# Kernel tuning notes

Measured on AMD Instinct MI355X. Metric: run time of the kernel, lower is better.

The kernel has to match this reference:

```python
import jax, jax.numpy as jnp
import numpy as np

NMS_THRESH = 0.5
SCORE_THRESH = 0.2
MAX_SUBJECT = 15
MAX_OBJECT = 15
B, NS, NO = 32, 512, 512


def _make_boxes(k, b, n):
    u = jax.random.uniform(k, (b, n, 4))
    xy = u[..., :2] * 1000.0          # top-left corner
    wh = u[..., 2:] * 200.0 + 1.0     # positive width/height
    return jnp.concatenate([xy, xy + wh], axis=-1)  # valid xyxy boxes


def setup_inputs() -> dict:
    key = jax.random.key(0)
    ks = jax.random.split(key, 6)
    return {
        "subj_boxes": _make_boxes(ks[0], B, NS),
        "subj_scores": jax.random.uniform(ks[1], (B, NS)),
        "subj_labels": jax.random.randint(ks[2], (B, NS), 0, 30, dtype=jnp.int32),
        "obj_boxes": _make_boxes(ks[3], B, NO),
        "obj_scores": jax.random.uniform(ks[4], (B, NO)),
        "obj_labels": jax.random.randint(ks[5], (B, NO), 0, 30, dtype=jnp.int32),
    }


def reference(subj_boxes, subj_scores, subj_labels, obj_boxes, obj_scores, obj_labels):
    # concat subject + object detections per image, as in preprocess()
    boxes = jnp.concatenate([subj_boxes, obj_boxes], axis=1)    # [B,N,4]
    scores = jnp.concatenate([subj_scores, obj_scores], axis=1) # [B,N]
    labels = jnp.concatenate([subj_labels, obj_labels], axis=1) # [B,N]
    b, n = scores.shape
    is_subj = jnp.arange(n) < subj_boxes.shape[1]               # [N]

    # sort by score descending (matches the argsort after NMS; greedy NMS
    # preserves this ordering among survivors)
    order = jnp.argsort(-scores, axis=1)
    boxes = jnp.take_along_axis(boxes, order[..., None], axis=1)
    scores = jnp.take_along_axis(scores, order, axis=1)
    labels = jnp.take_along_axis(labels, order, axis=1)
    is_subj = jnp.take(is_subj, order)                          # [B,N]

    active = scores >= SCORE_THRESH

    # torchvision batched_nms: offset boxes per class so distinct classes
    # never overlap (comparisons only -> no gradient path)
    max_coord = jax.lax.stop_gradient(jnp.max(boxes))
    ob = boxes + labels.astype(boxes.dtype)[..., None] * (max_coord + 1.0)

    # pairwise IoU [B,N,N]
    area = (ob[..., 2] - ob[..., 0]) * (ob[..., 3] - ob[..., 1])
    lt = jnp.maximum(ob[:, :, None, :2], ob[:, None, :, :2])
    rb = jnp.minimum(ob[:, :, None, 2:], ob[:, None, :, 2:])
    wh = jnp.clip(rb - lt, 0.0)
    inter = wh[..., 0] * wh[..., 1]
    iou = inter / (area[:, :, None] + area[:, None, :] - inter)

    later = jnp.arange(n)[None, :] > jnp.arange(n)[:, None]     # strictly lower-score

    def body(i, suppressed):  # greedy NMS, vectorized over batch
        keep_i = active[:, i] & ~suppressed[:, i]
        return suppressed | (keep_i[:, None] & (iou[:, i, :] > NMS_THRESH) & later[i])

    suppressed = jax.lax.fori_loop(0, n, body, jnp.zeros((b, n), dtype=bool))
    kept = active & ~suppressed

    # split survivors into subjects / objects, keep top max_subject/max_object
    neg = jnp.finfo(scores.dtype).min
    sub_key = jnp.where(kept & is_subj, scores, neg)
    obj_key = jnp.where(kept & ~is_subj, scores, neg)
    sv, si = jax.lax.top_k(sub_key, MAX_SUBJECT)
    ov, oi = jax.lax.top_k(obj_key, MAX_OBJECT)
    idx = jnp.concatenate([si, oi], axis=1)                     # [B,K]
    valid = jnp.concatenate([sv, ov], axis=1) > neg             # [B,K]

    out_boxes = jnp.take_along_axis(boxes, idx[..., None], axis=1) * valid[..., None]
    out_scores = jnp.take_along_axis(scores, idx, axis=1) * valid
    out_labels = jnp.where(valid, jnp.take_along_axis(labels, idx, axis=1), -1)
    num_subjects = jnp.sum(sv > neg, axis=1)
    return out_boxes, out_scores, out_labels, num_subjects, valid
```

## Files before the change

kernel.cpp:

```cpp
#include <hip/hip_runtime.h>
#include <stdint.h>

#define BQ    32
#define NSUB  512
#define NDET  1024
#define NCLS  30
#define KSLOT 30
#define CAP   128

#pragma clang fp contract(off)

typedef unsigned long long u64;

__global__ __launch_bounds__(1024) void max_kernel(
    const float4* __restrict__ sb4, const float4* __restrict__ ob4,
    unsigned* __restrict__ wsmax)
{
    int t = blockIdx.x * 1024 + threadIdx.x;
    float4 a = sb4[t], b = ob4[t];
    float m = fmaxf(fmaxf(fmaxf(a.x, a.y), fmaxf(a.z, a.w)),
                    fmaxf(fmaxf(b.x, b.y), fmaxf(b.z, b.w)));
    for (int off = 32; off; off >>= 1) m = fmaxf(m, __shfl_xor(m, off));
    if ((threadIdx.x & 63) == 0) atomicMax(wsmax, __float_as_uint(m));
}

__global__ __launch_bounds__(64) void nms_class_kernel(
    const float* __restrict__ sb, const float* __restrict__ ss,
    const int*   __restrict__ sl,
    const float* __restrict__ ob, const float* __restrict__ os,
    const int*   __restrict__ ol,
    const unsigned* __restrict__ wsmax,
    u64* __restrict__ subk, u64* __restrict__ objk)
{
#pragma clang fp contract(off)
    const int c    = blockIdx.x;
    const int b    = blockIdx.y;
    const int lane = threadIdx.x;

    __shared__ u64    keyarr[CAP];
    __shared__ u64    skey[CAP];
    __shared__ float4 bx4[CAP];

    const float mco  = __uint_as_float(wsmax[0]) + 1.0f;
    const float offc = (float)c * mco;

    int cnt = 0;
    for (int base = 0; base < NDET; base += 64) {
        int i = base + lane;
        float sc; int lb;
        if (i < NSUB) { sc = ss[b * NSUB + i];        lb = sl[b * NSUB + i]; }
        else          { sc = os[b * NSUB + i - NSUB]; lb = ol[b * NSUB + i - NSUB]; }
        bool pred = (lb == c) && (sc >= 0.2f);
        u64 mb = __ballot(pred);
        if (pred) {
            int pos = cnt + (int)__popcll(mb & ((1ull << lane) - 1ull));
            if (pos < CAP)
                keyarr[pos] = ((u64)__float_as_uint(sc) << 32) | (u64)(1023 - i);
        }
        cnt += (int)__popcll(mb);
    }
    if (cnt > CAP) cnt = CAP;
    __syncthreads();

    {
        u64 K = (lane < cnt) ? keyarr[lane] : 0;
        int r = 0;
        for (int l = 0; l < cnt; ++l) r += (keyarr[l] > K) ? 1 : 0;
        if (lane < cnt) skey[r] = K;
    }
    if (cnt > 64) {
        int e = 64 + lane;
        u64 K = (e < cnt) ? keyarr[e] : 0;
        int r = 0;
        for (int l = 0; l < cnt; ++l) r += (keyarr[l] > K) ? 1 : 0;
        if (e < cnt) skey[r] = K;
    }
    __syncthreads();

    const int lim1 = (cnt < 64) ? cnt : 64;
    const bool have1 = (lane < lim1);
    u64 SK1 = have1 ? skey[lane] : 0;
    int idx1 = 1023 - (int)(unsigned)(SK1 & 0xffffffffull);
    float4 bj1 = make_float4(0.f, 0.f, 0.f, 0.f);
    if (have1) {
        bj1 = (idx1 < NSUB)
            ? *(const float4*)(sb + (size_t)(b * NSUB + idx1) * 4)
            : *(const float4*)(ob + (size_t)(b * NSUB + idx1 - NSUB) * 4);
        bx4[lane] = bj1;
    }
    const bool have2 = (64 + lane) < cnt;
    u64 SK2 = 0; int idx2 = 0; float4 bj2 = make_float4(0.f, 0.f, 0.f, 0.f);
    if (cnt > 64) {
        SK2 = have2 ? skey[64 + lane] : 0;
        idx2 = 1023 - (int)(unsigned)(SK2 & 0xffffffffull);
        if (have2) {
            bj2 = (idx2 < NSUB)
                ? *(const float4*)(sb + (size_t)(b * NSUB + idx2) * 4)
                : *(const float4*)(ob + (size_t)(b * NSUB + idx2 - NSUB) * 4);
            bx4[64 + lane] = bj2;
        }
    }
    __syncthreads();

    float j0 = bj1.x + offc, j1 = bj1.y + offc, j2v = bj1.z + offc, j3 = bj1.w + offc;
    float aj = (j2v - j0) * (j3 - j1);
    u64 ov = 0;
    for (int l = 0; l < lim1; ++l) {
        float4 bl = bx4[l];
        float i0 = bl.x + offc, i1 = bl.y + offc, i2 = bl.z + offc, i3 = bl.w + offc;
        float ai = (i2 - i0) * (i3 - i1);
        if (have1 && l < lane) {
            float ltx = fmaxf(i0, j0), lty = fmaxf(i1, j1);
            float rbx = fminf(i2, j2v), rby = fminf(i3, j3);
            float wx = fmaxf(rbx - ltx, 0.0f), wy = fmaxf(rby - lty, 0.0f);
            float inter = wx * wy;
            float iou = inter / ((ai + aj) - inter);
            if (iou > 0.5f) ov |= (1ull << l);
        }
    }
    bool sup1 = !have1;
    for (int l = 0; l < lim1; ++l) {
        u64 bal = __ballot(sup1);
        if (!((bal >> l) & 1ull)) sup1 = sup1 || (((ov >> l) & 1ull) != 0ull);
    }
    const bool kept1 = have1 && !sup1;
    const u64 keptA = __ballot(kept1);

    bool kept2 = false;
    if (cnt > 64) {
        float k0 = bj2.x + offc, k1 = bj2.y + offc, k2 = bj2.z + offc, k3 = bj2.w + offc;
        float ak = (k2 - k0) * (k3 - k1);
        bool sup2 = !have2;
        for (int l = 0; l < 64; ++l) {
            if ((keptA >> l) & 1ull) {
                float4 bl = bx4[l];
                float i0 = bl.x + offc, i1 = bl.y + offc, i2 = bl.z + offc, i3 = bl.w + offc;
                float ai = (i2 - i0) * (i3 - i1);
                if (!sup2) {
                    float ltx = fmaxf(i0, k0), lty = fmaxf(i1, k1);
                    float rbx = fminf(i2, k2), rby = fminf(i3, k3);
                    float wx = fmaxf(rbx - ltx, 0.0f), wy = fmaxf(rby - lty, 0.0f);
                    float inter = wx * wy;
                    float iou = inter / ((ai + ak) - inter);
                    if (iou > 0.5f) sup2 = true;
                }
            }
        }
        u64 ov2 = 0;
        const int lim2 = cnt - 64;
        for (int l = 0; l < lim2; ++l) {
            float4 bl = bx4[64 + l];
            float i0 = bl.x + offc, i1 = bl.y + offc, i2 = bl.z + offc, i3 = bl.w + offc;
            float ai = (i2 - i0) * (i3 - i1);
            if (have2 && l < lane) {
                float ltx = fmaxf(i0, k0), lty = fmaxf(i1, k1);
                float rbx = fminf(i2, k2), rby = fminf(i3, k3);
                float wx = fmaxf(rbx - ltx, 0.0f), wy = fmaxf(rby - lty, 0.0f);
                float inter = wx * wy;
                float iou = inter / ((ai + ak) - inter);
                if (iou > 0.5f) ov2 |= (1ull << l);
            }
        }
        for (int l = 0; l < lim2; ++l) {
            u64 bal = __ballot(sup2);
            if (!((bal >> l) & 1ull)) sup2 = sup2 || (((ov2 >> l) & 1ull) != 0ull);
        }
        kept2 = have2 && !sup2;
    }

    const bool s1 = kept1 && (idx1 < NSUB), o1 = kept1 && (idx1 >= NSUB);
    const bool s2 = kept2 && (idx2 < NSUB), o2 = kept2 && (idx2 >= NSUB);
    const u64 mS1 = __ballot(s1), mS2 = __ballot(s2);
    const u64 mO1 = __ballot(o1), mO2 = __ballot(o2);
    const u64 ltm = (1ull << lane) - 1ull;
    u64* subp = subk + ((size_t)b * NCLS + c) * 15;
    u64* objp = objk + ((size_t)b * NCLS + c) * 15;
    if (s1) { int p = (int)__popcll(mS1 & ltm); if (p < 15) subp[p] = SK1; }
    if (s2) { int p = (int)__popcll(mS1) + (int)__popcll(mS2 & ltm); if (p < 15) subp[p] = SK2; }
    if (o1) { int p = (int)__popcll(mO1 & ltm); if (p < 15) objp[p] = SK1; }
    if (o2) { int p = (int)__popcll(mO1) + (int)__popcll(mO2 & ltm); if (p < 15) objp[p] = SK2; }
    int tS = (int)(__popcll(mS1) + __popcll(mS2)); if (tS > 15) tS = 15;
    int tO = (int)(__popcll(mO1) + __popcll(mO2)); if (tO > 15) tO = 15;
    if (lane >= tS && lane < 15) subp[lane] = 0;
    if (lane >= tO && lane < 15) objp[lane] = 0;
}

__global__ __launch_bounds__(512) void select_kernel(
    const float* __restrict__ sb, const float* __restrict__ ss,
    const int*   __restrict__ sl,
    const float* __restrict__ ob, const float* __restrict__ os,
    const int*   __restrict__ ol,
    const u64* __restrict__ subk, const u64* __restrict__ objk,
    float* __restrict__ out)
{
    const int b    = blockIdx.x;
    const int side = blockIdx.y;
    const int t    = threadIdx.x;
    __shared__ u64 ks[512];

    const u64* src = side ? objk : subk;
    u64 K = (t < NCLS * 15) ? src[(size_t)b * NCLS * 15 + t] : 0;

    for (unsigned k = 2; k <= 512; k <<= 1) {
        for (unsigned j = k >> 1; j > 0; j >>= 1) {
            bool want_max = (((t & k) == 0) == ((t & j) == 0));
            u64 other;
            if (j >= 64) {
                ks[t] = K; __syncthreads();
                other = ks[t ^ j]; __syncthreads();
            } else {
                other = __shfl_xor(K, (int)j);
            }
            bool take = want_max ? (other > K) : (other < K);
            if (take) K = other;
        }
    }

    float* outB = out;
    float* outS = out + BQ * KSLOT * 4;
    float* outL = outS + BQ * KSLOT;
    float* outN = outL + BQ * KSLOT;
    float* outV = outN + BQ;

    if (t < 15) {
        int p = b * KSLOT + (side ? (15 + t) : t);
        if (K != 0) {
            int idx = 1023 - (int)(unsigned)(K & 0xffffffffull);
            float score = __uint_as_float((unsigned)(K >> 32));
            float4 bx; int lb;
            if (idx < NSUB) {
                bx = *(const float4*)(sb + (size_t)(b * NSUB + idx) * 4);
                lb = sl[b * NSUB + idx];
            } else {
                bx = *(const float4*)(ob + (size_t)(b * NSUB + idx - NSUB) * 4);
                lb = ol[b * NSUB + idx - NSUB];
            }
            *(float4*)(outB + (size_t)p * 4) = bx;
            outS[p] = score;
            outL[p] = (float)lb;
            outV[p] = 1.0f;
        } else {
            *(float4*)(outB + (size_t)p * 4) = make_float4(0.f, 0.f, 0.f, 0.f);
            outS[p] = 0.0f;
            outL[p] = -1.0f;
            outV[p] = 0.0f;
        }
    }
    if (side == 0 && t < 64) {
        u64 mvalid = __ballot((t < 15) && (K != 0));
        if (t == 0) outN[b] = (float)__popcll(mvalid);
    }
}

extern "C" void kernel_launch(void* const* d_in, const int* in_sizes, int n_in,
                              void* d_out, int out_size, void* d_ws, size_t ws_size,
                              hipStream_t stream) {
    const float* sb = (const float*)d_in[0];
    const float* ss = (const float*)d_in[1];
    const int*   sl = (const int*)d_in[2];
    const float* ob = (const float*)d_in[3];
    const float* os = (const float*)d_in[4];
    const int*   ol = (const int*)d_in[5];

    unsigned* wsmax = (unsigned*)d_ws;
    u64* subk = (u64*)((char*)d_ws + 16);
    u64* objk = subk + (size_t)BQ * NCLS * 15;

    hipMemsetAsync(d_ws, 0, 16, stream);
    max_kernel<<<dim3(16), dim3(1024), 0, stream>>>(
        (const float4*)sb, (const float4*)ob, wsmax);
    nms_class_kernel<<<dim3(NCLS, BQ), dim3(64), 0, stream>>>(
        sb, ss, sl, ob, os, ol, wsmax, subk, objk);
    select_kernel<<<dim3(BQ, 2), dim3(512), 0, stream>>>(
        sb, ss, sl, ob, os, ol, subk, objk, (float*)d_out);
}
```

Measured before the change: 94.54 us.

## Fuse max, per-class NMS and top-k select into one per-image kernel

Replaces the memset and three kernels (global max, per-class NMS, bitonic select) with a single kernel of one 512-thread block per image. Each block recomputes the global box maximum redundantly, then its 8 wavefronts each handle classes in a strided loop, keeping candidates in shared memory before the bitonic top-k. This removes launch overhead and the global workspace round trip. In exchange, only 32 blocks run, each rereading all boxes for the max, and each wavefront processes about 4 classes serially, so parallelism drops.

```diff
diff --git a/kernel.cpp b/kernel.cpp
--- a/kernel.cpp
+++ b/kernel.cpp
@@ -7,214 +7,199 @@
 #define NCLS  30
 #define KSLOT 30
 #define CAP   128
+#define NTH   512
 
 #pragma clang fp contract(off)
 
 typedef unsigned long long u64;
 
-__global__ __launch_bounds__(1024) void max_kernel(
-    const float4* __restrict__ sb4, const float4* __restrict__ ob4,
-    unsigned* __restrict__ wsmax)
-{
-    int t = blockIdx.x * 1024 + threadIdx.x;
-    float4 a = sb4[t], b = ob4[t];
-    float m = fmaxf(fmaxf(fmaxf(a.x, a.y), fmaxf(a.z, a.w)),
-                    fmaxf(fmaxf(b.x, b.y), fmaxf(b.z, b.w)));
-    for (int off = 32; off; off >>= 1) m = fmaxf(m, __shfl_xor(m, off));
-    if ((threadIdx.x & 63) == 0) atomicMax(wsmax, __float_as_uint(m));
-}
-
-__global__ __launch_bounds__(64) void nms_class_kernel(
+__global__ __launch_bounds__(NTH) void fused_kernel(
     const float* __restrict__ sb, const float* __restrict__ ss,
     const int*   __restrict__ sl,
     const float* __restrict__ ob, const float* __restrict__ os,
     const int*   __restrict__ ol,
-    const unsigned* __restrict__ wsmax,
-    u64* __restrict__ subk, u64* __restrict__ objk)
+    float* __restrict__ out)
 {
 #pragma clang fp contract(off)
-    const int c    = blockIdx.x;
-    const int b    = blockIdx.y;
-    const int lane = threadIdx.x;
-
-    __shared__ u64    keyarr[CAP];
-    __shared__ u64    skey[CAP];
-    __shared__ float4 bx4[CAP];
-
-    const float mco  = __uint_as_float(wsmax[0]) + 1.0f;
-    const float offc = (float)c * mco;
-
-    int cnt = 0;
-    for (int base = 0; base < NDET; base += 64) {
-        int i = base + lane;
-        float sc; int lb;
-        if (i < NSUB) { sc = ss[b * NSUB + i];        lb = sl[b * NSUB + i]; }
-        else          { sc = os[b * NSUB + i - NSUB]; lb = ol[b * NSUB + i - NSUB]; }
-        bool pred = (lb == c) && (sc >= 0.2f);
-        u64 mb = __ballot(pred);
-        if (pred) {
-            int pos = cnt + (int)__popcll(mb & ((1ull << lane) - 1ull));
-            if (pos < CAP)
-                keyarr[pos] = ((u64)__float_as_uint(sc) << 32) | (u64)(1023 - i);
-        }
-        cnt += (int)__popcll(mb);
+    const int b    = blockIdx.x;
+    const int t    = threadIdx.x;
+    const int lane = t & 63;
+    const int w    = t >> 6;
+
+    __shared__ float  red[8];
+    __shared__ u64    keyarr[8][CAP];
+    __shared__ u64    skey[8][CAP];
+    __shared__ float4 bxw[8][CAP];
+    __shared__ u64    subcand[NTH];
+    __shared__ u64    objcand[NTH];
+    __shared__ u64    ks[NTH];
+
+    float m = 0.0f;
+    const float4* sb4 = (const float4*)sb;
+    const float4* ob4 = (const float4*)ob;
+    for (int i = t; i < BQ * NSUB; i += NTH) {
+        float4 a = sb4[i], c4 = ob4[i];
+        m = fmaxf(m, fmaxf(fmaxf(a.x, a.y), fmaxf(a.z, a.w)));
+        m = fmaxf(m, fmaxf(fmaxf(c4.x, c4.y), fmaxf(c4.z, c4.w)));
     }
-    if (cnt > CAP) cnt = CAP;
+    for (int off = 32; off; off >>= 1) m = fmaxf(m, __shfl_xor(m, off));
+    if (lane == 0) red[w] = m;
+    subcand[t] = 0;
+    objcand[t] = 0;
     __syncthreads();
-
-    {
-        u64 K = (lane < cnt) ? keyarr[lane] : 0;
-        int r = 0;
-        for (int l = 0; l < cnt; ++l) r += (keyarr[l] > K) ? 1 : 0;
-        if (lane < cnt) skey[r] = K;
-    }
-    if (cnt > 64) {
-        int e = 64 + lane;
-        u64 K = (e < cnt) ? keyarr[e] : 0;
-        int r = 0;
-        for (int l = 0; l < cnt; ++l) r += (keyarr[l] > K) ? 1 : 0;
-        if (e < cnt) skey[r] = K;
-    }
-    __syncthreads();
-
-    const int lim1 = (cnt < 64) ? cnt : 64;
-    const bool have1 = (lane < lim1);
-    u64 SK1 = have1 ? skey[lane] : 0;
-    int idx1 = 1023 - (int)(unsigned)(SK1 & 0xffffffffull);
-    float4 bj1 = make_float4(0.f, 0.f, 0.f, 0.f);
-    if (have1) {
-        bj1 = (idx1 < NSUB)
-            ? *(const float4*)(sb + (size_t)(b * NSUB + idx1) * 4)
-            : *(const float4*)(ob + (size_t)(b * NSUB + idx1 - NSUB) * 4);
-        bx4[lane] = bj1;
-    }
-    const bool have2 = (64 + lane) < cnt;
-    u64 SK2 = 0; int idx2 = 0; float4 bj2 = make_float4(0.f, 0.f, 0.f, 0.f);
-    if (cnt > 64) {
-        SK2 = have2 ? skey[64 + lane] : 0;
-        idx2 = 1023 - (int)(unsigned)(SK2 & 0xffffffffull);
-        if (have2) {
-            bj2 = (idx2 < NSUB)
-                ? *(const float4*)(sb + (size_t)(b * NSUB + idx2) * 4)
-                : *(const float4*)(ob + (size_t)(b * NSUB + idx2 - NSUB) * 4);
-            bx4[64 + lane] = bj2;
-        }
-    }
-    __syncthreads();
-
-    float j0 = bj1.x + offc, j1 = bj1.y + offc, j2v = bj1.z + offc, j3 = bj1.w + offc;
-    float aj = (j2v - j0) * (j3 - j1);
-    u64 ov = 0;
-    for (int l = 0; l < lim1; ++l) {
-        float4 bl = bx4[l];
-        float i0 = bl.x + offc, i1 = bl.y + offc, i2 = bl.z + offc, i3 = bl.w + offc;
-        float ai = (i2 - i0) * (i3 - i1);
-        if (have1 && l < lane) {
-            float ltx = fmaxf(i0, j0), lty = fmaxf(i1, j1);
-            float rbx = fminf(i2, j2v), rby = fminf(i3, j3);
-            float wx = fmaxf(rbx - ltx, 0.0f), wy = fmaxf(rby - lty, 0.0f);
-            float inter = wx * wy;
-            float iou = inter / ((ai + aj) - inter);
-            if (iou > 0.5f) ov |= (1ull << l);
-        }
-    }
-    bool sup1 = !have1;
-    for (int l = 0; l < lim1; ++l) {
-        u64 bal = __ballot(sup1);
-        if (!((bal >> l) & 1ull)) sup1 = sup1 || (((ov >> l) & 1ull) != 0ull);
-    }
-    const bool kept1 = have1 && !sup1;
-    const u64 keptA = __ballot(kept1);
-
-    bool kept2 = false;
-    if (cnt > 64) {
-        float k0 = bj2.x + offc, k1 = bj2.y + offc, k2 = bj2.z + offc, k3 = bj2.w + offc;
-        float ak = (k2 - k0) * (k3 - k1);
-        bool sup2 = !have2;
-        for (int l = 0; l < 64; ++l) {
-            if ((keptA >> l) & 1ull) {
-                float4 bl = bx4[l];
-                float i0 = bl.x + offc, i1 = bl.y + offc, i2 = bl.z + offc, i3 = bl.w + offc;
+    float mm = red[0];
+    for (int i = 1; i < 8; ++i) mm = fmaxf(mm, red[i]);
+    const float mco = mm + 1.0f;
+
+    for (int c = w; c < NCLS; c += 8) {
+        u64*    KA = keyarr[w];
+        u64*    SK = skey[w];
+        float4* BX = bxw[w];
+        const float offc = (float)c * mco;
+
+        int cnt = 0;
+        for (int base = 0; base < NDET; base += 64) {
+            int i = base + lane;
+            float scv; int lb;
+            if (i < NSUB) { scv = ss[b * NSUB + i];        lb = sl[b * NSUB + i]; }
+            else          { scv = os[b * NSUB + i - NSUB]; lb = ol[b * NSUB + i - NSUB]; }
+            bool pred = (lb == c) && (scv >= 0.2f);
+            u64 mb = __ballot(pred);
+            if (pred) {
+                int pos = cnt + (int)__popcll(mb & ((1ull << lane) - 1ull));
+                if (pos < CAP)
+                    KA[pos] = ((u64)__float_as_uint(scv) << 32) | (u64)(1023 - i);
+            }
+            cnt += (int)__popcll(mb);
+        }
+        if (cnt > CAP) cnt = CAP;
+        __threadfence_block();
+
+        {
+            u64 K = (lane < cnt) ? KA[lane] : 0;
+            int r = 0;
+            for (int l = 0; l < cnt; ++l) r += (KA[l] > K) ? 1 : 0;
+            if (lane < cnt) SK[r] = K;
+        }
+        if (cnt > 64) {
+            int e = 64 + lane;
+            u64 K = (e < cnt) ? KA[e] : 0;
+            int r = 0;
+            for (int l = 0; l < cnt; ++l) r += (KA[l] > K) ? 1 : 0;
+            if (e < cnt) SK[r] = K;
+        }
+        __threadfence_block();
+
+        const int  lim1  = (cnt < 64) ? cnt : 64;
+        const bool have1 = (lane < lim1);
+        u64 SK1 = have1 ? SK[lane] : 0;
+        int idx1 = 1023 - (int)(unsigned)(SK1 & 0xffffffffull);
+        float4 bj1 = make_float4(0.f, 0.f, 0.f, 0.f);
+        if (have1) {
+            bj1 = (idx1 < NSUB)
+                ? *(const float4*)(sb + (size_t)(b * NSUB + idx1) * 4)
+                : *(const float4*)(ob + (size_t)(b * NSUB + idx1 - NSUB) * 4);
+            BX[lane] = bj1;
+        }
+        const bool have2 = (64 + lane) < cnt;
+        u64 SK2 = 0; int idx2 = 0; float4 bj2 = make_float4(0.f, 0.f, 0.f, 0.f);
+        if (cnt > 64) {
+            SK2 = have2 ? SK[64 + lane] : 0;
+            idx2 = 1023 - (int)(unsigned)(SK2 & 0xffffffffull);
+            if (have2) {
+                bj2 = (idx2 < NSUB)
+                    ? *(const float4*)(sb + (size_t)(b * NSUB + idx2) * 4)
+                    : *(const float4*)(ob + (size_t)(b * NSUB + idx2 - NSUB) * 4);
+                BX[64 + lane] = bj2;
+            }
+        }
+        __threadfence_block();
+
+        float j0 = bj1.x + offc, j1 = bj1.y + offc;
+        float j2v = bj1.z + offc, j3 = bj1.w + offc;
+        float aj = (j2v - j0) * (j3 - j1);
+        u64 ov = 0;
+        for (int l = 0; l < lim1; ++l) {
+            float4 bl = BX[l];
+            float i0 = bl.x + offc, i1 = bl.y + offc;
+            float i2 = bl.z + offc, i3 = bl.w + offc;
+            float ai = (i2 - i0) * (i3 - i1);
+            if (have1 && l < lane) {
+                float ltx = fmaxf(i0, j0), lty = fmaxf(i1, j1);
+                float rbx = fminf(i2, j2v), rby = fminf(i3, j3);
+                float wx = fmaxf(rbx - ltx, 0.0f), wy = fmaxf(rby - lty, 0.0f);
+                float inter = wx * wy;
+                float iou = inter / ((ai + aj) - inter);
+                if (iou > 0.5f) ov |= (1ull << l);
+            }
+        }
+        bool sup1 = !have1;
+        for (int l = 0; l < lim1; ++l) {
+            u64 bal = __ballot(sup1);
+            if (!((bal >> l) & 1ull)) sup1 = sup1 || (((ov >> l) & 1ull) != 0ull);
+        }
+        const bool kept1 = have1 && !sup1;
+        const u64 keptA = __ballot(kept1);
+
+        bool kept2 = false;
+        if (cnt > 64) {
+            float k0 = bj2.x + offc, k1 = bj2.y + offc;
+            float k2 = bj2.z + offc, k3 = bj2.w + offc;
+            float ak = (k2 - k0) * (k3 - k1);
+            bool sup2 = !have2;
+            for (int l = 0; l < 64; ++l) {
+                if ((keptA >> l) & 1ull) {
+                    float4 bl = BX[l];
+                    float i0 = bl.x + offc, i1 = bl.y + offc;
+                    float i2 = bl.z + offc, i3 = bl.w + offc;
+                    float ai = (i2 - i0) * (i3 - i1);
+                    if (!sup2) {
+                        float ltx = fmaxf(i0, k0), lty = fmaxf(i1, k1);
+                        float rbx = fminf(i2, k2), rby = fminf(i3, k3);
+                        float wx = fmaxf(rbx - ltx, 0.0f), wy = fmaxf(rby - lty, 0.0f);
+                        float inter = wx * wy;
+                        float iou = inter / ((ai + ak) - inter);
+                        if (iou > 0.5f) sup2 = true;
+                    }
+                }
+            }
+            u64 ov2 = 0;
+            const int lim2 = cnt - 64;
+            for (int l = 0; l < lim2; ++l) {
+                float4 bl = BX[64 + l];
+                float i0 = bl.x + offc, i1 = bl.y + offc;
+                float i2 = bl.z + offc, i3 = bl.w + offc;
                 float ai = (i2 - i0) * (i3 - i1);
-                if (!sup2) {
+                if (have2 && l < lane) {
                     float ltx = fmaxf(i0, k0), lty = fmaxf(i1, k1);
                     float rbx = fminf(i2, k2), rby = fminf(i3, k3);
                     float wx = fmaxf(rbx - ltx, 0.0f), wy = fmaxf(rby - lty, 0.0f);
                     float inter = wx * wy;
                     float iou = inter / ((ai + ak) - inter);
-                    if (iou > 0.5f) sup2 = true;
-                }
-            }
-        }
-        u64 ov2 = 0;
-        const int lim2 = cnt - 64;
-        for (int l = 0; l < lim2; ++l) {
-            float4 bl = bx4[64 + l];
-            float i0 = bl.x + offc, i1 = bl.y + offc, i2 = bl.z + offc, i3 = bl.w + offc;
-            float ai = (i2 - i0) * (i3 - i1);
-            if (have2 && l < lane) {
-                float ltx = fmaxf(i0, k0), lty = fmaxf(i1, k1);
-                float rbx = fminf(i2, k2), rby = fminf(i3, k3);
-                float wx = fmaxf(rbx - ltx, 0.0f), wy = fmaxf(rby - lty, 0.0f);
-                float inter = wx * wy;
-                float iou = inter / ((ai + ak) - inter);
-                if (iou > 0.5f) ov2 |= (1ull << l);
-            }
-        }
-        for (int l = 0; l < lim2; ++l) {
-            u64 bal = __ballot(sup2);
-            if (!((bal >> l) & 1ull)) sup2 = sup2 || (((ov2 >> l) & 1ull) != 0ull);
-        }
-        kept2 = have2 && !sup2;
+                    if (iou > 0.5f) ov2 |= (1ull << l);
+                }
+            }
+            for (int l = 0; l < lim2; ++l) {
+                u64 bal = __ballot(sup2);
+                if (!((bal >> l) & 1ull)) sup2 = sup2 || (((ov2 >> l) & 1ull) != 0ull);
+            }
+            kept2 = have2 && !sup2;
+        }
+
+        const bool s1 = kept1 && (idx1 < NSUB), o1 = kept1 && (idx1 >= NSUB);
+        const bool s2 = kept2 && (idx2 < NSUB), o2 = kept2 && (idx2 >= NSUB);
+        const u64 mS1 = __ballot(s1), mS2 = __ballot(s2);
+        const u64 mO1 = __ballot(o1), mO2 = __ballot(o2);
+        const u64 ltm = (1ull << lane) - 1ull;
+        u64* subp = subcand + c * 15;
+        u64* objp = objcand + c * 15;
+        if (s1) { int p = (int)__popcll(mS1 & ltm); if (p < 15) subp[p] = SK1; }
+        if (s2) { int p = (int)__popcll(mS1) + (int)__popcll(mS2 & ltm); if (p < 15) subp[p] = SK2; }
+        if (o1) { int p = (int)__popcll(mO1 & ltm); if (p < 15) objp[p] = SK1; }
+        if (o2) { int p = (int)__popcll(mO1) + (int)__popcll(mO2 & ltm); if (p < 15) objp[p] = SK2; }
+        __threadfence_block();
     }
-
-    const bool s1 = kept1 && (idx1 < NSUB), o1 = kept1 && (idx1 >= NSUB);
-    const bool s2 = kept2 && (idx2 < NSUB), o2 = kept2 && (idx2 >= NSUB);
-    const u64 mS1 = __ballot(s1), mS2 = __ballot(s2);
-    const u64 mO1 = __ballot(o1), mO2 = __ballot(o2);
-    const u64 ltm = (1ull << lane) - 1ull;
-    u64* subp = subk + ((size_t)b * NCLS + c) * 15;
-    u64* objp = objk + ((size_t)b * NCLS + c) * 15;
-    if (s1) { int p = (int)__popcll(mS1 & ltm); if (p < 15) subp[p] = SK1; }
-    if (s2) { int p = (int)__popcll(mS1) + (int)__popcll(mS2 & ltm); if (p < 15) subp[p] = SK2; }
-    if (o1) { int p = (int)__popcll(mO1 & ltm); if (p < 15) objp[p] = SK1; }
-    if (o2) { int p = (int)__popcll(mO1) + (int)__popcll(mO2 & ltm); if (p < 15) objp[p] = SK2; }
-    int tS = (int)(__popcll(mS1) + __popcll(mS2)); if (tS > 15) tS = 15;
-    int tO = (int)(__popcll(mO1) + __popcll(mO2)); if (tO > 15) tO = 15;
-    if (lane >= tS && lane < 15) subp[lane] = 0;
-    if (lane >= tO && lane < 15) objp[lane] = 0;
-}
-
-__global__ __launch_bounds__(512) void select_kernel(
-    const float* __restrict__ sb, const float* __restrict__ ss,
-    const int*   __restrict__ sl,
-    const float* __restrict__ ob, const float* __restrict__ os,
-    const int*   __restrict__ ol,
-    const u64* __restrict__ subk, const u64* __restrict__ objk,
-    float* __restrict__ out)
-{
-    const int b    = blockIdx.x;
-    const int side = blockIdx.y;
-    const int t    = threadIdx.x;
-    __shared__ u64 ks[512];
-
-    const u64* src = side ? objk : subk;
-    u64 K = (t < NCLS * 15) ? src[(size_t)b * NCLS * 15 + t] : 0;
-
-    for (unsigned k = 2; k <= 512; k <<= 1) {
-        for (unsigned j = k >> 1; j > 0; j >>= 1) {
-            bool want_max = (((t & k) == 0) == ((t & j) == 0));
-            u64 other;
-            if (j >= 64) {
-                ks[t] = K; __syncthreads();
-                other = ks[t ^ j]; __syncthreads();
-            } else {
-                other = __shfl_xor(K, (int)j);
-            }
-            bool take = want_max ? (other > K) : (other < K);
-            if (take) K = other;
-        }
-    }
+    __syncthreads();
 
     float* outB = out;
     float* outS = out + BQ * KSLOT * 4;
@@ -222,33 +207,52 @@
     float* outN = outL + BQ * KSLOT;
     float* outV = outN + BQ;
 
-    if (t < 15) {
-        int p = b * KSLOT + (side ? (15 + t) : t);
-        if (K != 0) {
-            int idx = 1023 - (int)(unsigned)(K & 0xffffffffull);
-            float score = __uint_as_float((unsigned)(K >> 32));
-            float4 bx; int lb;
-            if (idx < NSUB) {
-                bx = *(const float4*)(sb + (size_t)(b * NSUB + idx) * 4);
-                lb = sl[b * NSUB + idx];
+    for (int side = 0; side < 2; ++side) {
+        u64 K = side ? objcand[t] : subcand[t];
+        for (unsigned k = 2; k <= NTH; k <<= 1) {
+            for (unsigned j = k >> 1; j > 0; j >>= 1) {
+                bool want_max = (((t & k) == 0) == ((t & j) == 0));
+                u64 other;
+                if (j >= 64) {
+                    ks[t] = K; __syncthreads();
+                    other = ks[t ^ j]; __syncthreads();
+                } else {
+                    other = __shfl_xor(K, (int)j);
+                }
+                bool take = want_max ? (other > K) : (other < K);
+                if (take) K = other;
+            }
+        }
+
+        if (t < 15) {
+            int p = b * KSLOT + (side ? (15 + t) : t);
+            if (K != 0) {
+                int idx = 1023 - (int)(unsigned)(K & 0xffffffffull);
+                float score = __uint_as_float((unsigned)(K >> 32));
+                float4 bx; int lb;
+                if (idx < NSUB) {
+                    bx = *(const float4*)(sb + (size_t)(b * NSUB + idx) * 4);
+                    lb = sl[b * NSUB + idx];
+                } else {
+                    bx = *(const float4*)(ob + (size_t)(b * NSUB + idx - NSUB) * 4);
+                    lb = ol[b * NSUB + idx - NSUB];
+                }
+                *(float4*)(outB + (size_t)p * 4) = bx;
+                outS[p] = score;
+                outL[p] = (float)lb;
+                outV[p] = 1.0f;
             } else {
-                bx = *(const float4*)(ob + (size_t)(b * NSUB + idx - NSUB) * 4);
-                lb = ol[b * NSUB + idx - NSUB];
-            }
-            *(float4*)(outB + (size_t)p * 4) = bx;
-            outS[p] = score;
-            outL[p] = (float)lb;
-            outV[p] = 1.0f;
-        } else {
-            *(float4*)(outB + (size_t)p * 4) = make_float4(0.f, 0.f, 0.f, 0.f);
-            outS[p] = 0.0f;
-            outL[p] = -1.0f;
-            outV[p] = 0.0f;
-        }
-    }
-    if (side == 0 && t < 64) {
-        u64 mvalid = __ballot((t < 15) && (K != 0));
-        if (t == 0) outN[b] = (float)__popcll(mvalid);
+                *(float4*)(outB + (size_t)p * 4) = make_float4(0.f, 0.f, 0.f, 0.f);
+                outS[p] = 0.0f;
+                outL[p] = -1.0f;
+                outV[p] = 0.0f;
+            }
+        }
+        if (side == 0 && t < 64) {
+            u64 mvalid = __ballot((t < 15) && (K != 0));
+            if (t == 0) outN[b] = (float)__popcll(mvalid);
+        }
+        __syncthreads();
     }
 }
 
@@ -261,16 +265,6 @@
     const float* ob = (const float*)d_in[3];
     const float* os = (const float*)d_in[4];
     const int*   ol = (const int*)d_in[5];
-
-    unsigned* wsmax = (unsigned*)d_ws;
-    u64* subk = (u64*)((char*)d_ws + 16);
-    u64* objk = subk + (size_t)BQ * NCLS * 15;
-
-    hipMemsetAsync(d_ws, 0, 16, stream);
-    max_kernel<<<dim3(16), dim3(1024), 0, stream>>>(
-        (const float4*)sb, (const float4*)ob, wsmax);
-    nms_class_kernel<<<dim3(NCLS, BQ), dim3(64), 0, stream>>>(
-        sb, ss, sl, ob, os, ol, wsmax, subk, objk);
-    select_kernel<<<dim3(BQ, 2), dim3(512), 0, stream>>>(
-        sb, ss, sl, ob, os, ol, subk, objk, (float*)d_out);
+    fused_kernel<<<dim3(BQ), dim3(NTH), 0, stream>>>(
+        sb, ss, sl, ob, os, ol, (float*)d_out);
 }
```

Result: slower. 121.4 us (+28.4%).

## Fuse top-k selection into NMS kernel via last-block atomic counter

Applied to the files above, without the earlier changes.

Drops the separate memset and select kernel. The max kernel now writes per-block partial maxima and resets per-image counters. The NMS kernel folds those partials itself, and the last class block to finish for each image does a wave-level iterative top-15 selection in place of the 512-thread bitonic sort. This removes two launches and a sort, at the cost of one atomic and a threadfence per block and a serial selection done by one wavefront per image.

```diff
diff --git a/kernel.cpp b/kernel.cpp
--- a/kernel.cpp
+++ b/kernel.cpp
@@ -14,14 +14,22 @@
 
 __global__ __launch_bounds__(1024) void max_kernel(
     const float4* __restrict__ sb4, const float4* __restrict__ ob4,
-    unsigned* __restrict__ wsmax)
+    float* __restrict__ pmax, int* __restrict__ done)
 {
-    int t = blockIdx.x * 1024 + threadIdx.x;
+    __shared__ float red[16];
+    const int t = blockIdx.x * 1024 + threadIdx.x;
     float4 a = sb4[t], b = ob4[t];
     float m = fmaxf(fmaxf(fmaxf(a.x, a.y), fmaxf(a.z, a.w)),
                     fmaxf(fmaxf(b.x, b.y), fmaxf(b.z, b.w)));
     for (int off = 32; off; off >>= 1) m = fmaxf(m, __shfl_xor(m, off));
-    if ((threadIdx.x & 63) == 0) atomicMax(wsmax, __float_as_uint(m));
+    if ((threadIdx.x & 63) == 0) red[threadIdx.x >> 6] = m;
+    __syncthreads();
+    if (threadIdx.x == 0) {
+        float mm = red[0];
+        for (int i = 1; i < 16; ++i) mm = fmaxf(mm, red[i]);
+        pmax[blockIdx.x] = mm;
+    }
+    if (blockIdx.x == 0 && threadIdx.x < BQ) done[threadIdx.x] = 0;
 }
 
 __global__ __launch_bounds__(64) void nms_class_kernel(
@@ -29,8 +37,9 @@
     const int*   __restrict__ sl,
     const float* __restrict__ ob, const float* __restrict__ os,
     const int*   __restrict__ ol,
-    const unsigned* __restrict__ wsmax,
-    u64* __restrict__ subk, u64* __restrict__ objk)
+    const float* __restrict__ pmax, int* __restrict__ done,
+    u64* __restrict__ subk, u64* __restrict__ objk,
+    float* __restrict__ out)
 {
 #pragma clang fp contract(off)
     const int c    = blockIdx.x;
@@ -41,7 +50,9 @@
     __shared__ u64    skey[CAP];
     __shared__ float4 bx4[CAP];
 
-    const float mco  = __uint_as_float(wsmax[0]) + 1.0f;
+    float mm = pmax[0];
+    for (int i = 1; i < 16; ++i) mm = fmaxf(mm, pmax[i]);
+    const float mco  = mm + 1.0f;
     const float offc = (float)c * mco;
 
     int cnt = 0;
@@ -77,7 +88,7 @@
     }
     __syncthreads();
 
-    const int lim1 = (cnt < 64) ? cnt : 64;
+    const int  lim1  = (cnt < 64) ? cnt : 64;
     const bool have1 = (lane < lim1);
     u64 SK1 = have1 ? skey[lane] : 0;
     int idx1 = 1023 - (int)(unsigned)(SK1 & 0xffffffffull);
@@ -102,12 +113,14 @@
     }
     __syncthreads();
 
-    float j0 = bj1.x + offc, j1 = bj1.y + offc, j2v = bj1.z + offc, j3 = bj1.w + offc;
+    float j0 = bj1.x + offc, j1 = bj1.y + offc;
+    float j2v = bj1.z + offc, j3 = bj1.w + offc;
     float aj = (j2v - j0) * (j3 - j1);
     u64 ov = 0;
     for (int l = 0; l < lim1; ++l) {
         float4 bl = bx4[l];
-        float i0 = bl.x + offc, i1 = bl.y + offc, i2 = bl.z + offc, i3 = bl.w + offc;
+        float i0 = bl.x + offc, i1 = bl.y + offc;
+        float i2 = bl.z + offc, i3 = bl.w + offc;
         float ai = (i2 - i0) * (i3 - i1);
         if (have1 && l < lane) {
             float ltx = fmaxf(i0, j0), lty = fmaxf(i1, j1);
@@ -128,13 +141,15 @@
 
     bool kept2 = false;
     if (cnt > 64) {
-        float k0 = bj2.x + offc, k1 = bj2.y + offc, k2 = bj2.z + offc, k3 = bj2.w + offc;
+        float k0 = bj2.x + offc, k1 = bj2.y + offc;
+        float k2 = bj2.z + offc, k3 = bj2.w + offc;
         float ak = (k2 - k0) * (k3 - k1);
         bool sup2 = !have2;
         for (int l = 0; l < 64; ++l) {
             if ((keptA >> l) & 1ull) {
                 float4 bl = bx4[l];
-                float i0 = bl.x + offc, i1 = bl.y + offc, i2 = bl.z + offc, i3 = bl.w + offc;
+                float i0 = bl.x + offc, i1 = bl.y + offc;
+                float i2 = bl.z + offc, i3 = bl.w + offc;
                 float ai = (i2 - i0) * (i3 - i1);
                 if (!sup2) {
                     float ltx = fmaxf(i0, k0), lty = fmaxf(i1, k1);
@@ -150,7 +165,8 @@
         const int lim2 = cnt - 64;
         for (int l = 0; l < lim2; ++l) {
             float4 bl = bx4[64 + l];
-            float i0 = bl.x + offc, i1 = bl.y + offc, i2 = bl.z + offc, i3 = bl.w + offc;
+            float i0 = bl.x + offc, i1 = bl.y + offc;
+            float i2 = bl.z + offc, i3 = bl.w + offc;
             float ai = (i2 - i0) * (i3 - i1);
             if (have2 && l < lane) {
                 float ltx = fmaxf(i0, k0), lty = fmaxf(i1, k1);
@@ -183,38 +199,14 @@
     int tO = (int)(__popcll(mO1) + __popcll(mO2)); if (tO > 15) tO = 15;
     if (lane >= tS && lane < 15) subp[lane] = 0;
     if (lane >= tO && lane < 15) objp[lane] = 0;
-}
-
-__global__ __launch_bounds__(512) void select_kernel(
-    const float* __restrict__ sb, const float* __restrict__ ss,
-    const int*   __restrict__ sl,
-    const float* __restrict__ ob, const float* __restrict__ os,
-    const int*   __restrict__ ol,
-    const u64* __restrict__ subk, const u64* __restrict__ objk,
-    float* __restrict__ out)
-{
-    const int b    = blockIdx.x;
-    const int side = blockIdx.y;
-    const int t    = threadIdx.x;
-    __shared__ u64 ks[512];
-
-    const u64* src = side ? objk : subk;
-    u64 K = (t < NCLS * 15) ? src[(size_t)b * NCLS * 15 + t] : 0;
-
-    for (unsigned k = 2; k <= 512; k <<= 1) {
-        for (unsigned j = k >> 1; j > 0; j >>= 1) {
-            bool want_max = (((t & k) == 0) == ((t & j) == 0));
-            u64 other;
-            if (j >= 64) {
-                ks[t] = K; __syncthreads();
-                other = ks[t ^ j]; __syncthreads();
-            } else {
-                other = __shfl_xor(K, (int)j);
-            }
-            bool take = want_max ? (other > K) : (other < K);
-            if (take) K = other;
-        }
-    }
+
+    __threadfence();
+    int old = 0;
+    if (lane == 0) old = atomicAdd(&done[b], 1);
+    old = __shfl(old, 0);
+    if (old != NCLS - 1) return;
+
+    __threadfence();
 
     float* outB = out;
     float* outS = out + BQ * KSLOT * 4;
@@ -222,33 +214,57 @@
     float* outN = outL + BQ * KSLOT;
     float* outV = outN + BQ;
 
-    if (t < 15) {
-        int p = b * KSLOT + (side ? (15 + t) : t);
-        if (K != 0) {
-            int idx = 1023 - (int)(unsigned)(K & 0xffffffffull);
-            float score = __uint_as_float((unsigned)(K >> 32));
-            float4 bx; int lb;
-            if (idx < NSUB) {
-                bx = *(const float4*)(sb + (size_t)(b * NSUB + idx) * 4);
-                lb = sl[b * NSUB + idx];
+    const u64* sk_im = subk + (size_t)b * NCLS * 15;
+    const u64* ok_im = objk + (size_t)b * NCLS * 15;
+
+    for (int side = 0; side < 2; ++side) {
+        const u64* src = side ? ok_im : sk_im;
+        u64 kk[8];
+        #pragma unroll
+        for (int i = 0; i < 8; ++i) {
+            int p = lane + 64 * i;
+            kk[i] = (p < NCLS * 15) ? src[p] : 0;
+        }
+        int nvalid = 0;
+        for (int r = 0; r < 15; ++r) {
+            u64 lm = 0; int li = 0;
+            #pragma unroll
+            for (int i = 0; i < 8; ++i) if (kk[i] > lm) { lm = kk[i]; li = i; }
+            u64 gm = lm;
+            for (int off = 32; off; off >>= 1) {
+                u64 o = __shfl_xor(gm, off);
+                if (o > gm) gm = o;
+            }
+            int p = b * KSLOT + (side ? (15 + r) : r);
+            if (gm == 0) {
+                if (lane == 0) {
+                    *(float4*)(outB + (size_t)p * 4) = make_float4(0.f, 0.f, 0.f, 0.f);
+                    outS[p] = 0.0f; outL[p] = -1.0f; outV[p] = 0.0f;
+                }
             } else {
-                bx = *(const float4*)(ob + (size_t)(b * NSUB + idx - NSUB) * 4);
-                lb = ol[b * NSUB + idx - NSUB];
-            }
-            *(float4*)(outB + (size_t)p * 4) = bx;
-            outS[p] = score;
-            outL[p] = (float)lb;
-            outV[p] = 1.0f;
-        } else {
-            *(float4*)(outB + (size_t)p * 4) = make_float4(0.f, 0.f, 0.f, 0.f);
-            outS[p] = 0.0f;
-            outL[p] = -1.0f;
-            outV[p] = 0.0f;
-        }
-    }
-    if (side == 0 && t < 64) {
-        u64 mvalid = __ballot((t < 15) && (K != 0));
-        if (t == 0) outN[b] = (float)__popcll(mvalid);
+                u64 win = __ballot(lm == gm);
+                int wl = (int)__ffsll(win) - 1;
+                if (lane == wl) {
+                    kk[li] = 0;
+                    int idx = 1023 - (int)(unsigned)(gm & 0xffffffffull);
+                    float score = __uint_as_float((unsigned)(gm >> 32));
+                    float4 bx; int lb;
+                    if (idx < NSUB) {
+                        bx = *(const float4*)(sb + (size_t)(b * NSUB + idx) * 4);
+                        lb = sl[b * NSUB + idx];
+                    } else {
+                        bx = *(const float4*)(ob + (size_t)(b * NSUB + idx - NSUB) * 4);
+                        lb = ol[b * NSUB + idx - NSUB];
+                    }
+                    *(float4*)(outB + (size_t)p * 4) = bx;
+                    outS[p] = score;
+                    outL[p] = (float)lb;
+                    outV[p] = 1.0f;
+                }
+                nvalid++;
+            }
+        }
+        if (side == 0 && lane == 0) outN[b] = (float)nvalid;
     }
 }
 
@@ -262,15 +278,13 @@
     const float* os = (const float*)d_in[4];
     const int*   ol = (const int*)d_in[5];
 
-    unsigned* wsmax = (unsigned*)d_ws;
-    u64* subk = (u64*)((char*)d_ws + 16);
-    u64* objk = subk + (size_t)BQ * NCLS * 15;
-
-    hipMemsetAsync(d_ws, 0, 16, stream);
+    float* pmax = (float*)d_ws;
+    int*   done = (int*)((char*)d_ws + 64);
+    u64*   subk = (u64*)((char*)d_ws + 256);
+    u64*   objk = subk + (size_t)BQ * NCLS * 15;
+
     max_kernel<<<dim3(16), dim3(1024), 0, stream>>>(
-        (const float4*)sb, (const float4*)ob, wsmax);
+        (const float4*)sb, (const float4*)ob, pmax, done);
     nms_class_kernel<<<dim3(NCLS, BQ), dim3(64), 0, stream>>>(
-        sb, ss, sl, ob, os, ol, wsmax, subk, objk);
-    select_kernel<<<dim3(BQ, 2), dim3(512), 0, stream>>>(
-        sb, ss, sl, ob, os, ol, subk, objk, (float*)d_out);
+        sb, ss, sl, ob, os, ol, pmax, done, subk, objk, (float*)d_out);
 }
```

Result: slower. 117.2 us (+24.0%).
